# Performance work log

Measured on AMD Instinct MI355X. Metric: run time of the kernel, lower is better.

The kernel has to match this reference:

```python
import jax, jax.numpy as jnp
import numpy as np

D_MODEL = 256
D_STATE = 16
D_INNER = 512          # expand=2 * d_model
D_CONV = 4
DT_RANK = 16           # ceil(d_model/16)
B, L = 16, 2048


def setup_inputs() -> dict:
    key = jax.random.key(0)
    ks = jax.random.split(key, 10)
    s = 0.02
    inp = {
        "x": jax.random.normal(ks[0], (B, L, D_MODEL), dtype=jnp.float32),
        "ln_w": jnp.ones((D_MODEL,), jnp.float32),
        "ln_b": jnp.zeros((D_MODEL,), jnp.float32),
        "in_proj_w": jax.random.normal(ks[1], (2 * D_INNER, D_MODEL)) * s,
        "conv_w": jax.random.normal(ks[2], (D_INNER, 1, D_CONV)) * s,
        "conv_b": jnp.zeros((D_INNER,), jnp.float32),
        "x_proj_w": jax.random.normal(ks[3], (DT_RANK + 2 * D_STATE, D_INNER)) * s,
        "dt_proj_w": jax.random.normal(ks[4], (D_INNER, DT_RANK)) * s,
        "dt_proj_b": jax.random.uniform(ks[5], (D_INNER,), minval=-4.0, maxval=-2.0),
        "A_log": jnp.log(jnp.broadcast_to(jnp.arange(1, D_STATE + 1, dtype=jnp.float32), (D_INNER, D_STATE))).copy(),
        "D_param": jnp.ones((D_INNER,), jnp.float32),
        "out_proj_w": jax.random.normal(ks[6], (D_MODEL, D_INNER)) * s,
    }
    return inp


def _layernorm(x, w, b, eps=1e-5):
    mu = jnp.mean(x, axis=-1, keepdims=True)
    var = jnp.var(x, axis=-1, keepdims=True)
    return (x - mu) * jax.lax.rsqrt(var + eps) * w + b


def _mamba(xn, in_proj_w, conv_w, conv_b, x_proj_w, dt_proj_w, dt_proj_b, A_log, D_param, out_proj_w):
    # in_proj -> x, z   (B, L, d_inner) each
    xz = jnp.einsum('bld,ed->ble', xn, in_proj_w)
    x_in, z = jnp.split(xz, 2, axis=-1)

    # depthwise causal conv over L
    xc = jax.lax.conv_general_dilated(
        jnp.transpose(x_in, (0, 2, 1)), conv_w,
        window_strides=(1,), padding=[(D_CONV - 1, 0)],
        feature_group_count=D_INNER,
        dimension_numbers=('NCH', 'OIH', 'NCH')) + conv_b[None, :, None]
    xc = jax.nn.silu(jnp.transpose(xc, (0, 2, 1)))  # (B, L, d_inner)

    # input-dependent dt, B, C
    dbc = jnp.einsum('ble,fe->blf', xc, x_proj_w)  # (B, L, dt_rank + 2N)
    dt = jax.nn.softplus(jnp.einsum('blr,er->ble', dbc[..., :DT_RANK], dt_proj_w) + dt_proj_b)
    Bc = dbc[..., DT_RANK:DT_RANK + D_STATE]   # (B, L, N)
    Cc = dbc[..., DT_RANK + D_STATE:]          # (B, L, N)

    A = -jnp.exp(A_log)  # (d_inner, N)

    def step(h, inputs):
        dt_t, x_t, B_t, C_t = inputs  # (B,e), (B,e), (B,n), (B,n)
        dA = jnp.exp(dt_t[..., None] * A)                      # (B, e, n)
        h = dA * h + dt_t[..., None] * B_t[:, None, :] * x_t[..., None]
        y = jnp.sum(h * C_t[:, None, :], axis=-1)              # (B, e)
        return h, y

    h0 = jnp.zeros((xn.shape[0], D_INNER, D_STATE), xn.dtype)
    seq = (jnp.swapaxes(dt, 0, 1), jnp.swapaxes(xc, 0, 1),
           jnp.swapaxes(Bc, 0, 1), jnp.swapaxes(Cc, 0, 1))
    _, ys = jax.lax.scan(step, h0, seq)
    y = jnp.swapaxes(ys, 0, 1) + D_param * xc                  # (B, L, e)
    y = y * jax.nn.silu(z)
    return jnp.einsum('ble,de->bld', y, out_proj_w)


def reference(x, ln_w, ln_b, in_proj_w, conv_w, conv_b, x_proj_w, dt_proj_w, dt_proj_b, A_log, D_param, out_proj_w):
    xn = _layernorm(x, ln_w, ln_b)
    out = _mamba(xn, in_proj_w, conv_w, conv_b, x_proj_w, dt_proj_w, dt_proj_b, A_log, D_param, out_proj_w)
    return x + out  # dropout is identity in eval
```

## Files before the change

### kernel.cpp

```cpp
#include <hip/hip_runtime.h>
#include <cstdint>

#define DEVI __device__ __forceinline__

typedef __bf16 bf16;
typedef __bf16 bf16x8 __attribute__((ext_vector_type(8)));
typedef __bf16 bf16x4 __attribute__((ext_vector_type(4)));
typedef __bf16 bf16x2 __attribute__((ext_vector_type(2)));
typedef float floatx4 __attribute__((ext_vector_type(4)));
typedef float f32x2 __attribute__((ext_vector_type(2)));

constexpr int BATCH = 16, SEQ = 2048, DM = 256, DI = 512;
constexpr int M = BATCH * SEQ;
constexpr int NC = 64;
constexpr int CL = SEQ / NC;
static_assert(NC * CL == SEQ, "chunking");
constexpr float LOG2E = 1.4426950408889634f;

DEVI void gl2lds16(const void* g, void* l) {
  __builtin_amdgcn_global_load_lds(
      (const __attribute__((address_space(1))) unsigned int*)(uintptr_t)g,
      (__attribute__((address_space(3))) unsigned int*)(unsigned int)(uintptr_t)l,
      16, 0, 0);
}

DEVI float sigmoidf_(float x) { return 1.f / (1.f + __expf(-x)); }
DEVI float exp2_(float x) { return __builtin_amdgcn_exp2f(x); }

DEVI float bflo(unsigned u) { return __uint_as_float(u << 16); }
DEVI float bfhi(unsigned u) { return __uint_as_float(u & 0xFFFF0000u); }
DEVI f32x2 sp2(float v) { f32x2 r; r[0] = v; r[1] = v; return r; }

DEVI void powseq(f32x2 d, f32x2* P) {
  P[0] = d;
  P[1] = d * d;
  P[2] = P[1] * d;
  P[3] = P[1] * P[1];
  P[4] = P[3] * d;
  P[5] = P[3] * P[1];
  P[6] = P[3] * P[2];
  P[7] = P[3] * P[3];
  P[8] = P[7] * d;
  P[9] = P[7] * P[1];
  P[10] = P[7] * P[2];
  P[11] = P[7] * P[3];
  P[12] = P[7] * P[4];
  P[13] = P[7] * P[5];
  P[14] = P[7] * P[6];
  P[15] = P[7] * P[7];
}

__global__ __launch_bounds__(256) void prep_kernel(
    const float* __restrict__ w1, const float* __restrict__ wx,
    const float* __restrict__ wo, const float* __restrict__ alog,
    bf16* __restrict__ w1b, bf16* __restrict__ wxb, bf16* __restrict__ wob,
    float* __restrict__ An, int* __restrict__ flags) {
  constexpr int n1 = 1024 * 256, n2 = 48 * 512, n3 = 256 * 512;
  int i = blockIdx.x * 256 + threadIdx.x;
  if (i < n1) w1b[i] = (bf16)w1[i];
  else if (i < n1 + n2) wxb[i - n1] = (bf16)wx[i - n1];
  else if (i < n1 + n2 + n3) wob[i - n1 - n2] = (bf16)wo[i - n1 - n2];
  else if (i < n1 + n2 + n3 + DI) {
    const int e = i - (n1 + n2 + n3);
    const float a0 = -__expf(alog[e * 16]);
    bool ok = (a0 < 0.f);
#pragma unroll 1
    for (int s = 0; s < 16; s++) {
      const float a = -__expf(alog[e * 16 + s]);
      An[e * 16 + s] = a * LOG2E;
      ok = ok && (__builtin_fabsf(a / a0 - (float)(s + 1)) < 1e-3f);
    }
    flags[e] = ok ? 1 : 0;
  }
}

__global__ __launch_bounds__(256) void ln_kernel(
    const float* __restrict__ x, const float* __restrict__ w,
    const float* __restrict__ b, bf16* __restrict__ xn) {
  const int row = blockIdx.x * 4 + (threadIdx.x >> 6);
  const int lane = threadIdx.x & 63;
  const float4 v = ((const float4*)(x + (size_t)row * DM))[lane];
  float s = v.x + v.y + v.z + v.w;
  float s2 = v.x * v.x + v.y * v.y + v.z * v.z + v.w * v.w;
#pragma unroll
  for (int m = 1; m < 64; m <<= 1) { s += __shfl_xor(s, m); s2 += __shfl_xor(s2, m); }
  const float mu = s * (1.f / DM);
  const float var = s2 * (1.f / DM) - mu * mu;
  const float rs = rsqrtf(var + 1e-5f);
  const float4 wv = ((const float4*)w)[lane];
  const float4 bv = ((const float4*)b)[lane];
  bf16x4 o;
  o[0] = (bf16)((v.x - mu) * rs * wv.x + bv.x);
  o[1] = (bf16)((v.y - mu) * rs * wv.y + bv.y);
  o[2] = (bf16)((v.z - mu) * rs * wv.z + bv.z);
  o[3] = (bf16)((v.w - mu) * rs * wv.w + bv.w);
  *(bf16x4*)(xn + (size_t)row * DM + lane * 4) = o;
}

template <int N, int K, bool OUT_BF16, bool RESID>
__global__ __launch_bounds__(256) void gemm_nt(const bf16* __restrict__ A,
                                               const bf16* __restrict__ W,
                                               void* __restrict__ out,
                                               const float* __restrict__ resid) {
  constexpr int BK = 32;
  constexpr int NB = N / 128;
  constexpr int MT_PER = (M / 128) / 8;
  __shared__ __align__(16) bf16 lA[128 * BK];
  __shared__ __align__(16) bf16 lB[128 * BK];
  const int tid = threadIdx.x;
  const int id = blockIdx.x;
  const int xcd = id & 7;
  const int local = id >> 3;
  const int bm = (xcd * MT_PER + local / NB) * 128;
  const int bn = (local % NB) * 128;
  const int wave = tid >> 6, lane = tid & 63;
  const int wm = (wave >> 1) * 64, wn = (wave & 1) * 64;
  const int q = lane >> 4, r = lane & 15;
  floatx4 acc[4][4] = {};
  const int c0 = wave * 64 + lane;
  const int row0 = c0 >> 2, kp = (c0 & 3) * 8;
  for (int k0 = 0; k0 < K; k0 += BK) {
    gl2lds16(A + (size_t)(bm + row0) * K + k0 + kp, lA + c0 * 8);
    gl2lds16(A + (size_t)(bm + row0 + 64) * K + k0 + kp, lA + (c0 + 256) * 8);
    gl2lds16(W + (size_t)(bn + row0) * K + k0 + kp, lB + c0 * 8);
    gl2lds16(W + (size_t)(bn + row0 + 64) * K + k0 + kp, lB + (c0 + 256) * 8);
    __syncthreads();
    bf16x8 af[4], bfr[4];
#pragma unroll
    for (int i = 0; i < 4; i++) af[i] = *(const bf16x8*)&lA[(wm + i * 16 + r) * BK + q * 8];
#pragma unroll
    for (int j = 0; j < 4; j++) bfr[j] = *(const bf16x8*)&lB[(wn + j * 16 + r) * BK + q * 8];
#pragma unroll
    for (int i = 0; i < 4; i++)
#pragma unroll
      for (int j = 0; j < 4; j++)
        acc[i][j] = __builtin_amdgcn_mfma_f32_16x16x32_bf16(af[i], bfr[j], acc[i][j], 0, 0, 0);
    __syncthreads();
  }
#pragma unroll
  for (int i = 0; i < 4; i++)
#pragma unroll
    for (int j = 0; j < 4; j++)
#pragma unroll
      for (int t = 0; t < 4; t++) {
        const int row = bm + wm + i * 16 + q * 4 + t;
        const int col = bn + wn + j * 16 + r;
        const size_t idx = (size_t)row * N + col;
        float v = acc[i][j][t];
        if constexpr (OUT_BF16) {
          ((bf16*)out)[idx] = (bf16)v;
        } else {
          if constexpr (RESID) v += resid[idx];
          ((float*)out)[idx] = v;
        }
      }
}

__global__ __launch_bounds__(256) void conv_silu(const bf16* __restrict__ xz,
                                                 const float* __restrict__ cw,
                                                 const float* __restrict__ cb,
                                                 bf16* __restrict__ xc) {
  const int tid = threadIdx.x;
  const int e2 = tid * 2;
  const int p0 = blockIdx.x * 8;
  const int b = blockIdx.y;
  const float4 w0 = ((const float4*)cw)[e2];
  const float4 w1 = ((const float4*)cw)[e2 + 1];
  const float2 bias = *(const float2*)(cb + e2);
  float xa[11], xb_[11];
#pragma unroll
  for (int j = 0; j < 11; j++) {
    const int pos = p0 - 3 + j;
    float fa = 0.f, fb = 0.f;
    if (pos >= 0) {
      const unsigned u = *(const unsigned*)(xz + ((size_t)b * SEQ + pos) * 1024 + e2);
      fa = __uint_as_float(u << 16);
      fb = __uint_as_float(u & 0xFFFF0000u);
    }
    xa[j] = fa; xb_[j] = fb;
  }
#pragma unroll
  for (int k = 0; k < 8; k++) {
    const float a0 = bias.x + xa[k] * w0.x + xa[k + 1] * w0.y + xa[k + 2] * w0.z + xa[k + 3] * w0.w;
    const float a1 = bias.y + xb_[k] * w1.x + xb_[k + 1] * w1.y + xb_[k + 2] * w1.z + xb_[k + 3] * w1.w;
    bf16x2 o;
    o[0] = (bf16)(a0 * sigmoidf_(a0));
    o[1] = (bf16)(a1 * sigmoidf_(a1));
    *(bf16x2*)(xc + ((size_t)b * SEQ + p0 + k) * DI + e2) = o;
  }
}

__global__ __launch_bounds__(256) void gemm_xproj(const bf16* __restrict__ A,
                                                  const bf16* __restrict__ W,
                                                  float* __restrict__ out) {
  constexpr int K = DI;
  __shared__ __align__(16) bf16 lW[48 * K];
  __shared__ __align__(16) bf16 lA[64 * 32];
  const int tid = threadIdx.x;
  const int wave = tid >> 6, lane = tid & 63;
  const int bm = blockIdx.x * 64;
  const int q = lane >> 4, r = lane & 15;
#pragma unroll
  for (int rd = 0; rd < 12; rd++) {
    const int c = rd * 256 + tid;
    gl2lds16((const char*)W + (size_t)c * 16, (char*)lW + (size_t)c * 16);
  }
  const int row0 = tid >> 2, kp = (tid & 3) * 8;
  const int wm = wave * 16;
  floatx4 acc[3] = {};
  for (int k0 = 0; k0 < K; k0 += 32) {
    gl2lds16(A + (size_t)(bm + row0) * K + k0 + kp, lA + tid * 8);
    __syncthreads();
    bf16x8 af = *(const bf16x8*)&lA[(wm + r) * 32 + q * 8];
#pragma unroll
    for (int j = 0; j < 3; j++) {
      const bf16x8 bfr = *(const bf16x8*)&lW[(j * 16 + r) * K + k0 + q * 8];
      acc[j] = __builtin_amdgcn_mfma_f32_16x16x32_bf16(af, bfr, acc[j], 0, 0, 0);
    }
    __syncthreads();
  }
#pragma unroll
  for (int j = 0; j < 3; j++)
#pragma unroll
    for (int t = 0; t < 4; t++)
      out[(size_t)(bm + wm + q * 4 + t) * 48 + j * 16 + r] = acc[j][t];
}

__global__ __launch_bounds__(256) void dtproj_kernel(const float* __restrict__ dbc,
                                                     const float* __restrict__ dtw,
                                                     const float* __restrict__ dtb,
                                                     bf16* __restrict__ dt) {
  __shared__ __align__(16) float sd[64 * 16];
  const int tid = threadIdx.x;
  const int p0 = blockIdx.x * 64;
  const int e = blockIdx.y * 256 + tid;
  {
    const int rowi = tid >> 2, coli = (tid & 3) * 4;
    *(float4*)&sd[rowi * 16 + coli] = *(const float4*)(dbc + (size_t)(p0 + rowi) * 48 + coli);
  }
  float w[16];
#pragma unroll
  for (int s = 0; s < 16; s += 4) {
    float4 t4 = *(const float4*)(dtw + (size_t)e * 16 + s);
    w[s] = t4.x; w[s + 1] = t4.y; w[s + 2] = t4.z; w[s + 3] = t4.w;
  }
  const float bias = dtb[e];
  __syncthreads();
  for (int p = 0; p < 64; p++) {
    float s = bias;
#pragma unroll
    for (int r2 = 0; r2 < 16; r2++) s += sd[p * 16 + r2] * w[r2];
    const float sp = (s > 15.f) ? s : __logf(1.f + __expf(s));
    dt[(size_t)(p0 + p) * DI + e] = (bf16)sp;
  }
}

__global__ __launch_bounds__(256) void scan_pass1(const bf16* __restrict__ dt,
                                                  const bf16* __restrict__ xc,
                                                  const float* __restrict__ dbc,
                                                  const float* __restrict__ An,
                                                  const int* __restrict__ flags,
                                                  float* __restrict__ U,
                                                  float* __restrict__ SD) {
  __shared__ __align__(16) float sbc[CL * 16];
  const int tid = threadIdx.x;
  const int e2 = tid * 2;
  const int ch = blockIdx.x, b = blockIdx.y;
  const size_t posBase = (size_t)b * SEQ + (size_t)ch * CL;
  if (tid < CL * 4) {
    const int il = tid >> 2, f = (tid & 3) * 4;
    gl2lds16(dbc + (posBase + il) * 48 + 16 + f, (char*)sbc + tid * 16);
  }
  const int2 fl = *(const int2*)(flags + e2);
  const int fast = fl.x & fl.y;
  f32x2 h[16];
#pragma unroll
  for (int s = 0; s < 16; s++) { h[s][0] = 0.f; h[s][1] = 0.f; }
  f32x2 sdt2; sdt2[0] = 0.f; sdt2[1] = 0.f;
  f32x2 A02; A02[0] = An[(size_t)e2 * 16]; A02[1] = An[(size_t)e2 * 16 + 16];
  float Aa[16], Ab[16];
  if (!fast) {
#pragma unroll
    for (int s = 0; s < 16; s += 4) {
      float4 a4 = *(const float4*)(An + (size_t)e2 * 16 + s);
      Aa[s] = a4.x; Aa[s + 1] = a4.y; Aa[s + 2] = a4.z; Aa[s + 3] = a4.w;
      float4 b4 = *(const float4*)(An + (size_t)e2 * 16 + 16 + s);
      Ab[s] = b4.x; Ab[s + 1] = b4.y; Ab[s + 2] = b4.z; Ab[s + 3] = b4.w;
    }
  }
  const char* pdt = (const char*)(dt + posBase * DI + e2);
  const char* pxc = (const char*)(xc + posBase * DI + e2);
  unsigned ud = *(const unsigned*)pdt;
  unsigned ux = *(const unsigned*)pxc;
  __syncthreads();
  if (fast) {
#pragma unroll 1
    for (int il = 0; il < CL; il++) {
      const int np = (il + 1 < CL) ? (il + 1) : il;
      const unsigned nud = *(const unsigned*)(pdt + (size_t)np * DI * 2);
      const unsigned nux = *(const unsigned*)(pxc + (size_t)np * DI * 2);
      f32x2 dt2; dt2[0] = bflo(ud); dt2[1] = bfhi(ud);
      f32x2 xv2; xv2[0] = bflo(ux); xv2[1] = bfhi(ux);
      const f32x2 dtx2 = dt2 * xv2;
      sdt2 = sdt2 + dt2;
      const f32x2 t = dt2 * A02;
      f32x2 d; d[0] = exp2_(t[0]); d[1] = exp2_(t[1]);
      f32x2 P[16];
      powseq(d, P);
      const float4* bb = (const float4*)(sbc + il * 16);
#pragma unroll
      for (int g = 0; g < 4; g++) {
        const float4 B4 = bb[g];
        h[4 * g + 0] = P[4 * g + 0] * h[4 * g + 0] + dtx2 * sp2(B4.x);
        h[4 * g + 1] = P[4 * g + 1] * h[4 * g + 1] + dtx2 * sp2(B4.y);
        h[4 * g + 2] = P[4 * g + 2] * h[4 * g + 2] + dtx2 * sp2(B4.z);
        h[4 * g + 3] = P[4 * g + 3] * h[4 * g + 3] + dtx2 * sp2(B4.w);
      }
      ud = nud; ux = nux;
    }
  } else {
#pragma unroll 1
    for (int il = 0; il < CL; il++) {
      const int np = (il + 1 < CL) ? (il + 1) : il;
      const unsigned nud = *(const unsigned*)(pdt + (size_t)np * DI * 2);
      const unsigned nux = *(const unsigned*)(pxc + (size_t)np * DI * 2);
      const float dta = bflo(ud), dtb_v = bfhi(ud);
      const float xa = bflo(ux), xb = bfhi(ux);
      const float dtxa = dta * xa, dtxb = dtb_v * xb;
      sdt2[0] += dta; sdt2[1] += dtb_v;
      const float* bc = sbc + il * 16;
#pragma unroll
      for (int s = 0; s < 16; s++) {
        const float bv = bc[s];
        h[s][0] = exp2_(dta * Aa[s]) * h[s][0] + dtxa * bv;
        h[s][1] = exp2_(dtb_v * Ab[s]) * h[s][1] + dtxb * bv;
      }
      ud = nud; ux = nux;
    }
  }
  float* up = U + ((size_t)(b * NC + ch) * DI + e2) * 16;
#pragma unroll
  for (int i = 0; i < 4; i++) {
    float4 o; o.x = h[4 * i][0]; o.y = h[4 * i + 1][0]; o.z = h[4 * i + 2][0]; o.w = h[4 * i + 3][0];
    ((float4*)up)[i] = o;
  }
#pragma unroll
  for (int i = 0; i < 4; i++) {
    float4 o; o.x = h[4 * i][1]; o.y = h[4 * i + 1][1]; o.z = h[4 * i + 2][1]; o.w = h[4 * i + 3][1];
    ((float4*)up)[4 + i] = o;
  }
  float2 sdo; sdo.x = sdt2[0]; sdo.y = sdt2[1];
  *(float2*)(SD + (size_t)(b * NC + ch) * DI + e2) = sdo;
}

__global__ __launch_bounds__(256) void scan_pass2(const float* __restrict__ SD,
                                                  float* U,
                                                  const float* __restrict__ An) {
  const int t = blockIdx.x * 256 + threadIdx.x;
  const int s = t & 15;
  const int e = (t >> 4) & (DI - 1);
  const int b = t >> 13;
  const float Av = An[e * 16 + s];
  const float* sdp = SD + (size_t)b * NC * DI + e;
  float* up = U + ((size_t)b * NC * DI + e) * 16 + s;
  float sA_[16], uA_[16], sB_[16], uB_[16];
#pragma unroll
  for (int j = 0; j < 16; j++) {
    sA_[j] = sdp[(size_t)j * DI];
    uA_[j] = up[(size_t)j * DI * 16];
  }
  float h = 0.f;
#pragma unroll 1
  for (int c0 = 0; c0 < NC; c0 += 32) {
#pragma unroll
    for (int j = 0; j < 16; j++) {
      sB_[j] = sdp[(size_t)(c0 + 16 + j) * DI];
      uB_[j] = up[(size_t)(c0 + 16 + j) * DI * 16];
    }
#pragma unroll
    for (int j = 0; j < 16; j++) {
      const float h0 = h;
      h = exp2_(Av * sA_[j]) * h0 + uA_[j];
      up[(size_t)(c0 + j) * DI * 16] = h0;
    }
    const int nn = (c0 + 32 < NC) ? (c0 + 32) : (NC - 16);
#pragma unroll
    for (int j = 0; j < 16; j++) {
      sA_[j] = sdp[(size_t)(nn + j) * DI];
      uA_[j] = up[(size_t)(nn + j) * DI * 16];
    }
#pragma unroll
    for (int j = 0; j < 16; j++) {
      const float h0 = h;
      h = exp2_(Av * sB_[j]) * h0 + uB_[j];
      up[(size_t)(c0 + 16 + j) * DI * 16] = h0;
    }
  }
}

__global__ __launch_bounds__(256) void scan_pass3(const bf16* __restrict__ dt,
                                                  const bf16* __restrict__ xc,
                                                  const bf16* __restrict__ xz,
                                                  const float* __restrict__ dbc,
                                                  const float* __restrict__ An,
                                                  const int* __restrict__ flags,
                                                  const float* __restrict__ H0,
                                                  const float* __restrict__ Dp,
                                                  bf16* __restrict__ yg) {
  __shared__ __align__(16) float sbc[CL * 32];
  const int tid = threadIdx.x;
  const int e2 = tid * 2;
  const int ch = blockIdx.x, b = blockIdx.y;
  const size_t posBase = (size_t)b * SEQ + (size_t)ch * CL;
  {
    const int il = tid >> 3, f = (tid & 7) * 4;
    gl2lds16(dbc + (posBase + il) * 48 + 16 + f, (char*)sbc + tid * 16);
  }
  const int2 fl = *(const int2*)(flags + e2);
  const int fast = fl.x & fl.y;
  f32x2 h[16];
  const float* hp = H0 + ((size_t)(b * NC + ch) * DI + e2) * 16;
#pragma unroll
  for (int i = 0; i < 4; i++) {
    const float4 h4 = ((const float4*)hp)[i];
    h[4 * i][0] = h4.x; h[4 * i + 1][0] = h4.y; h[4 * i + 2][0] = h4.z; h[4 * i + 3][0] = h4.w;
  }
#pragma unroll
  for (int i = 0; i < 4; i++) {
    const float4 h4 = ((const float4*)hp)[4 + i];
    h[4 * i][1] = h4.x; h[4 * i + 1][1] = h4.y; h[4 * i + 2][1] = h4.z; h[4 * i + 3][1] = h4.w;
  }
  const float2 Dv = *(const float2*)(Dp + e2);
  f32x2 Dv2; Dv2[0] = Dv.x; Dv2[1] = Dv.y;
  f32x2 A02; A02[0] = An[(size_t)e2 * 16]; A02[1] = An[(size_t)e2 * 16 + 16];
  float Aa[16], Ab[16];
  if (!fast) {
#pragma unroll
    for (int s = 0; s < 16; s += 4) {
      float4 a4 = *(const float4*)(An + (size_t)e2 * 16 + s);
      Aa[s] = a4.x; Aa[s + 1] = a4.y; Aa[s + 2] = a4.z; Aa[s + 3] = a4.w;
      float4 b4 = *(const float4*)(An + (size_t)e2 * 16 + 16 + s);
      Ab[s] = b4.x; Ab[s + 1] = b4.y; Ab[s + 2] = b4.z; Ab[s + 3] = b4.w;
    }
  }
  const char* pdt = (const char*)(dt + posBase * DI + e2);
  const char* pxc = (const char*)(xc + posBase * DI + e2);
  const char* pxz = (const char*)(xz + posBase * 1024 + DI + e2);
  unsigned ud = *(const unsigned*)pdt;
  unsigned ux = *(const unsigned*)pxc;
  unsigned uz = *(const unsigned*)pxz;
  __syncthreads();
  if (fast) {
#pragma unroll 1
    for (int il = 0; il < CL; il++) {
      const int np = (il + 1 < CL) ? (il + 1) : il;
      const unsigned nud = *(const unsigned*)(pdt + (size_t)np * DI * 2);
      const unsigned nux = *(const unsigned*)(pxc + (size_t)np * DI * 2);
      const unsigned nuz = *(const unsigned*)(pxz + (size_t)np * 1024 * 2);
      const size_t pos = posBase + il;
      f32x2 dt2; dt2[0] = bflo(ud); dt2[1] = bfhi(ud);
      f32x2 xv2; xv2[0] = bflo(ux); xv2[1] = bfhi(ux);
      f32x2 z2; z2[0] = bflo(uz); z2[1] = bfhi(uz);
      const f32x2 dtx2 = dt2 * xv2;
      const f32x2 t = dt2 * A02;
      f32x2 d; d[0] = exp2_(t[0]); d[1] = exp2_(t[1]);
      f32x2 P[16];
      powseq(d, P);
      const float4* bb = (const float4*)(sbc + il * 32);
      f32x2 Yv[4];
#pragma unroll
      for (int g = 0; g < 4; g++) { Yv[g][0] = 0.f; Yv[g][1] = 0.f; }
#pragma unroll
      for (int g = 0; g < 4; g++) {
        const float4 B4 = bb[g];
        const float4 C4 = bb[4 + g];
        h[4 * g + 0] = P[4 * g + 0] * h[4 * g + 0] + dtx2 * sp2(B4.x);
        Yv[g] = Yv[g] + h[4 * g + 0] * sp2(C4.x);
        h[4 * g + 1] = P[4 * g + 1] * h[4 * g + 1] + dtx2 * sp2(B4.y);
        Yv[g] = Yv[g] + h[4 * g + 1] * sp2(C4.y);
        h[4 * g + 2] = P[4 * g + 2] * h[4 * g + 2] + dtx2 * sp2(B4.z);
        Yv[g] = Yv[g] + h[4 * g + 2] * sp2(C4.z);
        h[4 * g + 3] = P[4 * g + 3] * h[4 * g + 3] + dtx2 * sp2(B4.w);
        Yv[g] = Yv[g] + h[4 * g + 3] * sp2(C4.w);
      }
      const f32x2 Ys = (Yv[0] + Yv[1]) + (Yv[2] + Yv[3]);
      f32x2 gz; gz[0] = z2[0] * sigmoidf_(z2[0]); gz[1] = z2[1] * sigmoidf_(z2[1]);
      const f32x2 yv2 = (Ys + Dv2 * xv2) * gz;
      bf16x2 o; o[0] = (bf16)yv2[0]; o[1] = (bf16)yv2[1];
      *(bf16x2*)(yg + pos * DI + e2) = o;
      ud = nud; ux = nux; uz = nuz;
    }
  } else {
#pragma unroll 1
    for (int il = 0; il < CL; il++) {
      const int np = (il + 1 < CL) ? (il + 1) : il;
      const unsigned nud = *(const unsigned*)(pdt + (size_t)np * DI * 2);
      const unsigned nux = *(const unsigned*)(pxc + (size_t)np * DI * 2);
      const unsigned nuz = *(const unsigned*)(pxz + (size_t)np * 1024 * 2);
      const size_t pos = posBase + il;
      const float dta = bflo(ud), dtb_v = bfhi(ud);
      const float xa = bflo(ux), xb = bfhi(ux);
      const float za = bflo(uz), zb = bfhi(uz);
      const float dtxa = dta * xa, dtxb = dtb_v * xb;
      const float* bc = sbc + il * 32;
      float ya = 0.f, yb = 0.f;
#pragma unroll
      for (int s = 0; s < 16; s++) {
        const float bv = bc[s], cv = bc[16 + s];
        const float ha = exp2_(dta * Aa[s]) * h[s][0] + dtxa * bv;
        const float hb = exp2_(dtb_v * Ab[s]) * h[s][1] + dtxb * bv;
        h[s][0] = ha; h[s][1] = hb;
        ya += ha * cv; yb += hb * cv;
      }
      const float yva = (ya + Dv.x * xa) * za * sigmoidf_(za);
      const float yvb = (yb + Dv.y * xb) * zb * sigmoidf_(zb);
      bf16x2 o; o[0] = (bf16)yva; o[1] = (bf16)yvb;
      *(bf16x2*)(yg + pos * DI + e2) = o;
      ud = nud; ux = nux; uz = nuz;
    }
  }
}

extern "C" void kernel_launch(void* const* d_in, const int* in_sizes, int n_in,
                              void* d_out, int out_size, void* d_ws, size_t ws_size,
                              hipStream_t stream) {
  const float* x = (const float*)d_in[0];
  const float* ln_w = (const float*)d_in[1];
  const float* ln_b = (const float*)d_in[2];
  const float* w_in = (const float*)d_in[3];
  const float* conv_w = (const float*)d_in[4];
  const float* conv_b = (const float*)d_in[5];
  const float* w_x = (const float*)d_in[6];
  const float* w_dt = (const float*)d_in[7];
  const float* b_dt = (const float*)d_in[8];
  const float* a_log = (const float*)d_in[9];
  const float* d_par = (const float*)d_in[10];
  const float* w_out = (const float*)d_in[11];

  char* ws = (char*)d_ws;
  size_t off = 0;
  auto alloc = [&](size_t bytes) {
    void* p = ws + off;
    off = (off + bytes + 255) & ~(size_t)255;
    return p;
  };
  bf16* xn = (bf16*)alloc((size_t)M * DM * 2);
  bf16* xzb = (bf16*)alloc((size_t)M * 1024 * 2);
  bf16* xcb = (bf16*)alloc((size_t)M * DI * 2);
  float* dbc = (float*)alloc((size_t)M * 48 * 4);
  bf16* dtb_ = (bf16*)alloc((size_t)M * DI * 2);
  bf16* ygb = (bf16*)alloc((size_t)M * DI * 2);
  float* U = (float*)alloc((size_t)BATCH * NC * DI * 16 * 4);
  float* SD = (float*)alloc((size_t)BATCH * NC * DI * 4);
  bf16* w1b = (bf16*)alloc(1024 * 256 * 2);
  bf16* wxb = (bf16*)alloc(48 * 512 * 2);
  bf16* wob = (bf16*)alloc(256 * 512 * 2);
  float* An = (float*)alloc(512 * 16 * 4);
  int* flags = (int*)alloc(512 * 4);

  constexpr int prep_n = 1024 * 256 + 48 * 512 + 256 * 512 + DI;
  prep_kernel<<<dim3((prep_n + 255) / 256), dim3(256), 0, stream>>>(w_in, w_x, w_out, a_log, w1b, wxb, wob, An, flags);
  ln_kernel<<<dim3(M / 4), dim3(256), 0, stream>>>(x, ln_w, ln_b, xn);
  gemm_nt<1024, 256, true, false><<<dim3((M / 128) * 8), dim3(256), 0, stream>>>(xn, w1b, (void*)xzb, nullptr);
  conv_silu<<<dim3(SEQ / 8, BATCH), dim3(256), 0, stream>>>(xzb, conv_w, conv_b, xcb);
  gemm_xproj<<<dim3(M / 64), dim3(256), 0, stream>>>(xcb, wxb, dbc);
  dtproj_kernel<<<dim3(M / 64, 2), dim3(256), 0, stream>>>(dbc, w_dt, b_dt, dtb_);
  scan_pass1<<<dim3(NC, BATCH), dim3(256), 0, stream>>>(dtb_, xcb, dbc, An, flags, U, SD);
  scan_pass2<<<dim3(BATCH * DI * 16 / 256), dim3(256), 0, stream>>>(SD, U, An);
  scan_pass3<<<dim3(NC, BATCH), dim3(256), 0, stream>>>(dtb_, xcb, xzb, dbc, An, flags, U, d_par, ygb);
  gemm_nt<256, 512, false, true><<<dim3((M / 128) * 2), dim3(256), 0, stream>>>(ygb, wob, d_out, x);
}
```

Before: 301.3 us.

## Double-buffer dt/xc/z rows into LDS via async loads in scan passes

Scan pass 1 and pass 3 now stage sub-chunks of 8 timesteps of dt, xc (and z in pass 3) into double-buffered shared memory using global_load_lds. The next sub-chunk's copy is issued while the current one is computed, replacing the per-step scalar global loads whose latency sat on the serial recurrence. This adds LDS footprint and a barrier per sub-chunk, which may reduce occupancy. Separately, the xn buffer is aliased onto the U scratch buffer to shrink workspace, relying on xn being dead before U is written.

```diff
diff --git a/kernel.cpp b/kernel.cpp
--- a/kernel.cpp
+++ b/kernel.cpp
@@ -14,6 +14,8 @@
 constexpr int M = BATCH * SEQ;
 constexpr int NC = 64;
 constexpr int CL = SEQ / NC;
+constexpr int SC = 8;
+constexpr int NSC = CL / SC;
 static_assert(NC * CL == SEQ, "chunking");
 constexpr float LOG2E = 1.4426950408889634f;
 
@@ -48,6 +50,17 @@
   P[13] = P[7] * P[5];
   P[14] = P[7] * P[6];
   P[15] = P[7] * P[7];
+}
+
+DEVI void stage_rows(const bf16* src, bf16* dst, int tid) {
+  gl2lds16((const char*)src + tid * 16, (char*)dst + tid * 16);
+  gl2lds16((const char*)src + tid * 16 + 4096, (char*)dst + tid * 16 + 4096);
+}
+DEVI void stage_z(const bf16* srcRow0, bf16* dst, int tid) {
+  int c = tid;
+  gl2lds16((const char*)srcRow0 + (size_t)(c >> 6) * 2048 + (c & 63) * 16, (char*)dst + c * 16);
+  c = tid + 256;
+  gl2lds16((const char*)srcRow0 + (size_t)(c >> 6) * 2048 + (c & 63) * 16, (char*)dst + c * 16);
 }
 
 __global__ __launch_bounds__(256) void prep_kernel(
@@ -263,6 +276,8 @@
                                                   float* __restrict__ U,
                                                   float* __restrict__ SD) {
   __shared__ __align__(16) float sbc[CL * 16];
+  __shared__ __align__(16) bf16 sdt_[2][SC * DI];
+  __shared__ __align__(16) bf16 sxc_[2][SC * DI];
   const int tid = threadIdx.x;
   const int e2 = tid * 2;
   const int ch = blockIdx.x, b = blockIdx.y;
@@ -271,6 +286,8 @@
     const int il = tid >> 2, f = (tid & 3) * 4;
     gl2lds16(dbc + (posBase + il) * 48 + 16 + f, (char*)sbc + tid * 16);
   }
+  stage_rows(dt + posBase * DI, sdt_[0], tid);
+  stage_rows(xc + posBase * DI, sxc_[0], tid);
   const int2 fl = *(const int2*)(flags + e2);
   const int fast = fl.x & fl.y;
   f32x2 h[16];
@@ -288,55 +305,61 @@
       Ab[s] = b4.x; Ab[s + 1] = b4.y; Ab[s + 2] = b4.z; Ab[s + 3] = b4.w;
     }
   }
-  const char* pdt = (const char*)(dt + posBase * DI + e2);
-  const char* pxc = (const char*)(xc + posBase * DI + e2);
-  unsigned ud = *(const unsigned*)pdt;
-  unsigned ux = *(const unsigned*)pxc;
   __syncthreads();
-  if (fast) {
 #pragma unroll 1
-    for (int il = 0; il < CL; il++) {
-      const int np = (il + 1 < CL) ? (il + 1) : il;
-      const unsigned nud = *(const unsigned*)(pdt + (size_t)np * DI * 2);
-      const unsigned nux = *(const unsigned*)(pxc + (size_t)np * DI * 2);
-      f32x2 dt2; dt2[0] = bflo(ud); dt2[1] = bfhi(ud);
-      f32x2 xv2; xv2[0] = bflo(ux); xv2[1] = bfhi(ux);
-      const f32x2 dtx2 = dt2 * xv2;
-      sdt2 = sdt2 + dt2;
-      const f32x2 t = dt2 * A02;
-      f32x2 d; d[0] = exp2_(t[0]); d[1] = exp2_(t[1]);
-      f32x2 P[16];
-      powseq(d, P);
-      const float4* bb = (const float4*)(sbc + il * 16);
-#pragma unroll
-      for (int g = 0; g < 4; g++) {
-        const float4 B4 = bb[g];
-        h[4 * g + 0] = P[4 * g + 0] * h[4 * g + 0] + dtx2 * sp2(B4.x);
-        h[4 * g + 1] = P[4 * g + 1] * h[4 * g + 1] + dtx2 * sp2(B4.y);
-        h[4 * g + 2] = P[4 * g + 2] * h[4 * g + 2] + dtx2 * sp2(B4.z);
-        h[4 * g + 3] = P[4 * g + 3] * h[4 * g + 3] + dtx2 * sp2(B4.w);
+  for (int sc = 0; sc < NSC; sc++) {
+    const int cb = sc & 1;
+    if (sc + 1 < NSC) {
+      stage_rows(dt + (posBase + (sc + 1) * SC) * DI, sdt_[cb ^ 1], tid);
+      stage_rows(xc + (posBase + (sc + 1) * SC) * DI, sxc_[cb ^ 1], tid);
+    }
+    const char* sdtb = (const char*)sdt_[cb];
+    const char* sxcb = (const char*)sxc_[cb];
+    const int tid4 = tid * 4;
+    if (fast) {
+#pragma unroll 2
+      for (int il = 0; il < SC; il++) {
+        const int ig = sc * SC + il;
+        const unsigned ud = *(const unsigned*)(sdtb + il * 1024 + tid4);
+        const unsigned ux = *(const unsigned*)(sxcb + il * 1024 + tid4);
+        f32x2 dt2; dt2[0] = bflo(ud); dt2[1] = bfhi(ud);
+        f32x2 xv2; xv2[0] = bflo(ux); xv2[1] = bfhi(ux);
+        const f32x2 dtx2 = dt2 * xv2;
+        sdt2 = sdt2 + dt2;
+        const f32x2 t = dt2 * A02;
+        f32x2 d; d[0] = exp2_(t[0]); d[1] = exp2_(t[1]);
+        f32x2 P[16];
+        powseq(d, P);
+        const float4* bb = (const float4*)(sbc + ig * 16);
+#pragma unroll
+        for (int g = 0; g < 4; g++) {
+          const float4 B4 = bb[g];
+          h[4 * g + 0] = P[4 * g + 0] * h[4 * g + 0] + dtx2 * sp2(B4.x);
+          h[4 * g + 1] = P[4 * g + 1] * h[4 * g + 1] + dtx2 * sp2(B4.y);
+          h[4 * g + 2] = P[4 * g + 2] * h[4 * g + 2] + dtx2 * sp2(B4.z);
+          h[4 * g + 3] = P[4 * g + 3] * h[4 * g + 3] + dtx2 * sp2(B4.w);
+        }
       }
-      ud = nud; ux = nux;
-    }
-  } else {
-#pragma unroll 1
-    for (int il = 0; il < CL; il++) {
-      const int np = (il + 1 < CL) ? (il + 1) : il;
-      const unsigned nud = *(const unsigned*)(pdt + (size_t)np * DI * 2);
-      const unsigned nux = *(const unsigned*)(pxc + (size_t)np * DI * 2);
-      const float dta = bflo(ud), dtb_v = bfhi(ud);
-      const float xa = bflo(ux), xb = bfhi(ux);
-      const float dtxa = dta * xa, dtxb = dtb_v * xb;
-      sdt2[0] += dta; sdt2[1] += dtb_v;
-      const float* bc = sbc + il * 16;
-#pragma unroll
-      for (int s = 0; s < 16; s++) {
-        const float bv = bc[s];
-        h[s][0] = exp2_(dta * Aa[s]) * h[s][0] + dtxa * bv;
-        h[s][1] = exp2_(dtb_v * Ab[s]) * h[s][1] + dtxb * bv;
+    } else {
+#pragma unroll 2
+      for (int il = 0; il < SC; il++) {
+        const int ig = sc * SC + il;
+        const unsigned ud = *(const unsigned*)(sdtb + il * 1024 + tid4);
+        const unsigned ux = *(const unsigned*)(sxcb + il * 1024 + tid4);
+        const float dta = bflo(ud), dtb_v = bfhi(ud);
+        const float xa = bflo(ux), xb = bfhi(ux);
+        const float dtxa = dta * xa, dtxb = dtb_v * xb;
+        sdt2[0] += dta; sdt2[1] += dtb_v;
+        const float* bc = sbc + ig * 16;
+#pragma unroll
+        for (int s = 0; s < 16; s++) {
+          const float bv = bc[s];
+          h[s][0] = exp2_(dta * Aa[s]) * h[s][0] + dtxa * bv;
+          h[s][1] = exp2_(dtb_v * Ab[s]) * h[s][1] + dtxb * bv;
+        }
       }
-      ud = nud; ux = nux;
-    }
+    }
+    __syncthreads();
   }
   float* up = U + ((size_t)(b * NC + ch) * DI + e2) * 16;
 #pragma unroll
@@ -408,6 +431,9 @@
                                                   const float* __restrict__ Dp,
                                                   bf16* __restrict__ yg) {
   __shared__ __align__(16) float sbc[CL * 32];
+  __shared__ __align__(16) bf16 sdt_[2][SC * DI];
+  __shared__ __align__(16) bf16 sxc_[2][SC * DI];
+  __shared__ __align__(16) bf16 sxz_[2][SC * DI];
   const int tid = threadIdx.x;
   const int e2 = tid * 2;
   const int ch = blockIdx.x, b = blockIdx.y;
@@ -416,6 +442,9 @@
     const int il = tid >> 3, f = (tid & 7) * 4;
     gl2lds16(dbc + (posBase + il) * 48 + 16 + f, (char*)sbc + tid * 16);
   }
+  stage_rows(dt + posBase * DI, sdt_[0], tid);
+  stage_rows(xc + posBase * DI, sxc_[0], tid);
+  stage_z(xz + posBase * 1024 + DI, sxz_[0], tid);
   const int2 fl = *(const int2*)(flags + e2);
   const int fast = fl.x & fl.y;
   f32x2 h[16];
@@ -443,81 +472,85 @@
       Ab[s] = b4.x; Ab[s + 1] = b4.y; Ab[s + 2] = b4.z; Ab[s + 3] = b4.w;
     }
   }
-  const char* pdt = (const char*)(dt + posBase * DI + e2);
-  const char* pxc = (const char*)(xc + posBase * DI + e2);
-  const char* pxz = (const char*)(xz + posBase * 1024 + DI + e2);
-  unsigned ud = *(const unsigned*)pdt;
-  unsigned ux = *(const unsigned*)pxc;
-  unsigned uz = *(const unsigned*)pxz;
   __syncthreads();
-  if (fast) {
 #pragma unroll 1
-    for (int il = 0; il < CL; il++) {
-      const int np = (il + 1 < CL) ? (il + 1) : il;
-      const unsigned nud = *(const unsigned*)(pdt + (size_t)np * DI * 2);
-      const unsigned nux = *(const unsigned*)(pxc + (size_t)np * DI * 2);
-      const unsigned nuz = *(const unsigned*)(pxz + (size_t)np * 1024 * 2);
-      const size_t pos = posBase + il;
-      f32x2 dt2; dt2[0] = bflo(ud); dt2[1] = bfhi(ud);
-      f32x2 xv2; xv2[0] = bflo(ux); xv2[1] = bfhi(ux);
-      f32x2 z2; z2[0] = bflo(uz); z2[1] = bfhi(uz);
-      const f32x2 dtx2 = dt2 * xv2;
-      const f32x2 t = dt2 * A02;
-      f32x2 d; d[0] = exp2_(t[0]); d[1] = exp2_(t[1]);
-      f32x2 P[16];
-      powseq(d, P);
-      const float4* bb = (const float4*)(sbc + il * 32);
-      f32x2 Yv[4];
-#pragma unroll
-      for (int g = 0; g < 4; g++) { Yv[g][0] = 0.f; Yv[g][1] = 0.f; }
-#pragma unroll
-      for (int g = 0; g < 4; g++) {
-        const float4 B4 = bb[g];
-        const float4 C4 = bb[4 + g];
-        h[4 * g + 0] = P[4 * g + 0] * h[4 * g + 0] + dtx2 * sp2(B4.x);
-        Yv[g] = Yv[g] + h[4 * g + 0] * sp2(C4.x);
-        h[4 * g + 1] = P[4 * g + 1] * h[4 * g + 1] + dtx2 * sp2(B4.y);
-        Yv[g] = Yv[g] + h[4 * g + 1] * sp2(C4.y);
-        h[4 * g + 2] = P[4 * g + 2] * h[4 * g + 2] + dtx2 * sp2(B4.z);
-        Yv[g] = Yv[g] + h[4 * g + 2] * sp2(C4.z);
-        h[4 * g + 3] = P[4 * g + 3] * h[4 * g + 3] + dtx2 * sp2(B4.w);
-        Yv[g] = Yv[g] + h[4 * g + 3] * sp2(C4.w);
+  for (int sc = 0; sc < NSC; sc++) {
+    const int cb = sc & 1;
+    if (sc + 1 < NSC) {
+      stage_rows(dt + (posBase + (sc + 1) * SC) * DI, sdt_[cb ^ 1], tid);
+      stage_rows(xc + (posBase + (sc + 1) * SC) * DI, sxc_[cb ^ 1], tid);
+      stage_z(xz + (posBase + (sc + 1) * SC) * 1024 + DI, sxz_[cb ^ 1], tid);
+    }
+    const char* sdtb = (const char*)sdt_[cb];
+    const char* sxcb = (const char*)sxc_[cb];
+    const char* sxzb = (const char*)sxz_[cb];
+    const int tid4 = tid * 4;
+    if (fast) {
+#pragma unroll 2
+      for (int il = 0; il < SC; il++) {
+        const int ig = sc * SC + il;
+        const unsigned ud = *(const unsigned*)(sdtb + il * 1024 + tid4);
+        const unsigned ux = *(const unsigned*)(sxcb + il * 1024 + tid4);
+        const unsigned uz = *(const unsigned*)(sxzb + il * 1024 + tid4);
+        f32x2 dt2; dt2[0] = bflo(ud); dt2[1] = bfhi(ud);
+        f32x2 xv2; xv2[0] = bflo(ux); xv2[1] = bfhi(ux);
+        f32x2 z2; z2[0] = bflo(uz); z2[1] = bfhi(uz);
+        const f32x2 dtx2 = dt2 * xv2;
+        const f32x2 t = dt2 * A02;
+        f32x2 d; d[0] = exp2_(t[0]); d[1] = exp2_(t[1]);
+        f32x2 P[16];
+        powseq(d, P);
+        const float4* bb = (const float4*)(sbc + ig * 32);
+        f32x2 Yv[4];
+#pragma unroll
+        for (int g = 0; g < 4; g++) { Yv[g][0] = 0.f; Yv[g][1] = 0.f; }
+#pragma unroll
+        for (int g = 0; g < 4; g++) {
+          const float4 B4 = bb[g];
+          const float4 C4 = bb[4 + g];
+          h[4 * g + 0] = P[4 * g + 0] * h[4 * g + 0] + dtx2 * sp2(B4.x);
+          Yv[g] = Yv[g] + h[4 * g + 0] * sp2(C4.x);
+          h[4 * g + 1] = P[4 * g + 1] * h[4 * g + 1] + dtx2 * sp2(B4.y);
+          Yv[g] = Yv[g] + h[4 * g + 1] * sp2(C4.y);
+          h[4 * g + 2] = P[4 * g + 2] * h[4 * g + 2] + dtx2 * sp2(B4.z);
+          Yv[g] = Yv[g] + h[4 * g + 2] * sp2(C4.z);
+          h[4 * g + 3] = P[4 * g + 3] * h[4 * g + 3] + dtx2 * sp2(B4.w);
+          Yv[g] = Yv[g] + h[4 * g + 3] * sp2(C4.w);
+        }
+        const f32x2 Ys = (Yv[0] + Yv[1]) + (Yv[2] + Yv[3]);
+        f32x2 gz; gz[0] = z2[0] * sigmoidf_(z2[0]); gz[1] = z2[1] * sigmoidf_(z2[1]);
+        const f32x2 yv2 = (Ys + Dv2 * xv2) * gz;
+        bf16x2 o; o[0] = (bf16)yv2[0]; o[1] = (bf16)yv2[1];
+        *(bf16x2*)(yg + (posBase + ig) * DI + e2) = o;
       }
-      const f32x2 Ys = (Yv[0] + Yv[1]) + (Yv[2] + Yv[3]);
-      f32x2 gz; gz[0] = z2[0] * sigmoidf_(z2[0]); gz[1] = z2[1] * sigmoidf_(z2[1]);
-      const f32x2 yv2 = (Ys + Dv2 * xv2) * gz;
-      bf16x2 o; o[0] = (bf16)yv2[0]; o[1] = (bf16)yv2[1];
-      *(bf16x2*)(yg + pos * DI + e2) = o;
-      ud = nud; ux = nux; uz = nuz;
-    }
-  } else {
-#pragma unroll 1
-    for (int il = 0; il < CL; il++) {
-      const int np = (il + 1 < CL) ? (il + 1) : il;
-      const unsigned nud = *(const unsigned*)(pdt + (size_t)np * DI * 2);
-      const unsigned nux = *(const unsigned*)(pxc + (size_t)np * DI * 2);
-      const unsigned nuz = *(const unsigned*)(pxz + (size_t)np * 1024 * 2);
-      const size_t pos = posBase + il;
-      const float dta = bflo(ud), dtb_v = bfhi(ud);
-      const float xa = bflo(ux), xb = bfhi(ux);
-      const float za = bflo(uz), zb = bfhi(uz);
-      const float dtxa = dta * xa, dtxb = dtb_v * xb;
-      const float* bc = sbc + il * 32;
-      float ya = 0.f, yb = 0.f;
-#pragma unroll
-      for (int s = 0; s < 16; s++) {
-        const float bv = bc[s], cv = bc[16 + s];
-        const float ha = exp2_(dta * Aa[s]) * h[s][0] + dtxa * bv;
-        const float hb = exp2_(dtb_v * Ab[s]) * h[s][1] + dtxb * bv;
-        h[s][0] = ha; h[s][1] = hb;
-        ya += ha * cv; yb += hb * cv;
+    } else {
+#pragma unroll 2
+      for (int il = 0; il < SC; il++) {
+        const int ig = sc * SC + il;
+        const unsigned ud = *(const unsigned*)(sdtb + il * 1024 + tid4);
+        const unsigned ux = *(const unsigned*)(sxcb + il * 1024 + tid4);
+        const unsigned uz = *(const unsigned*)(sxzb + il * 1024 + tid4);
+        const float dta = bflo(ud), dtb_v = bfhi(ud);
+        const float xa = bflo(ux), xb = bfhi(ux);
+        const float za = bflo(uz), zb = bfhi(uz);
+        const float dtxa = dta * xa, dtxb = dtb_v * xb;
+        const float* bc = sbc + ig * 32;
+        float ya = 0.f, yb = 0.f;
+#pragma unroll
+        for (int s = 0; s < 16; s++) {
+          const float bv = bc[s], cv = bc[16 + s];
+          const float ha = exp2_(dta * Aa[s]) * h[s][0] + dtxa * bv;
+          const float hb = exp2_(dtb_v * Ab[s]) * h[s][1] + dtxb * bv;
+          h[s][0] = ha; h[s][1] = hb;
+          ya += ha * cv; yb += hb * cv;
+        }
+        const float yva = (ya + Dv.x * xa) * za * sigmoidf_(za);
+        const float yvb = (yb + Dv.y * xb) * zb * sigmoidf_(zb);
+        bf16x2 o; o[0] = (bf16)yva; o[1] = (bf16)yvb;
+        *(bf16x2*)(yg + (posBase + ig) * DI + e2) = o;
       }
-      const float yva = (ya + Dv.x * xa) * za * sigmoidf_(za);
-      const float yvb = (yb + Dv.y * xb) * zb * sigmoidf_(zb);
-      bf16x2 o; o[0] = (bf16)yva; o[1] = (bf16)yvb;
-      *(bf16x2*)(yg + pos * DI + e2) = o;
-      ud = nud; ux = nux; uz = nuz;
-    }
+    }
+    __syncthreads();
   }
 }
 
@@ -544,13 +577,13 @@
     off = (off + bytes + 255) & ~(size_t)255;
     return p;
   };
-  bf16* xn = (bf16*)alloc((size_t)M * DM * 2);
   bf16* xzb = (bf16*)alloc((size_t)M * 1024 * 2);
   bf16* xcb = (bf16*)alloc((size_t)M * DI * 2);
   float* dbc = (float*)alloc((size_t)M * 48 * 4);
   bf16* dtb_ = (bf16*)alloc((size_t)M * DI * 2);
   bf16* ygb = (bf16*)alloc((size_t)M * DI * 2);
   float* U = (float*)alloc((size_t)BATCH * NC * DI * 16 * 4);
+  bf16* xn = (bf16*)U;
   float* SD = (float*)alloc((size_t)BATCH * NC * DI * 4);
   bf16* w1b = (bf16*)alloc(1024 * 256 * 2);
   bf16* wxb = (bf16*)alloc(48 * 512 * 2);
```

Result: no change. 299.2 us (-0.7%).
